# Performance work log

Hardware: AMD Instinct MI355X
Metric: run time of the kernel (lower is better)

The kernel has to match this reference:

```python
import jax, jax.numpy as jnp
import numpy as np

D = 768
NH = 12
HD = D // NH
N_MLP = 3072
LN_EPS = 1e-6


def layer_norm(x, g, b, eps=LN_EPS):
    mu = jnp.mean(x, axis=-1, keepdims=True)
    var = jnp.mean(jnp.square(x - mu), axis=-1, keepdims=True)
    return (x - mu) * jax.lax.rsqrt(var + eps) * g + b


def setup_inputs() -> dict:
    key = jax.random.key(0)
    ks = jax.random.split(key, 6)
    x = jax.random.normal(ks[0], (2, 4096, D), dtype=jnp.float32)
    # torch Linear weights are (out, in); init std=0.02, zero bias
    W_qkv = 0.02 * jax.random.normal(ks[1], (3 * D, D), dtype=jnp.float32)
    b_qkv = jnp.zeros((3 * D,), dtype=jnp.float32)
    W_proj = 0.02 * jax.random.normal(ks[2], (D, D), dtype=jnp.float32)
    b_proj = jnp.zeros((D,), dtype=jnp.float32)
    W1 = 0.02 * jax.random.normal(ks[3], (N_MLP, D), dtype=jnp.float32)
    b1 = jnp.zeros((N_MLP,), dtype=jnp.float32)
    W2 = 0.02 * jax.random.normal(ks[4], (D, N_MLP), dtype=jnp.float32)
    b2 = jnp.zeros((D,), dtype=jnp.float32)
    g1 = jnp.ones((D,), dtype=jnp.float32)
    beta1 = jnp.zeros((D,), dtype=jnp.float32)
    g2 = jnp.ones((D,), dtype=jnp.float32)
    beta2 = jnp.zeros((D,), dtype=jnp.float32)
    return dict(x=x, W_qkv=W_qkv, b_qkv=b_qkv, W_proj=W_proj, b_proj=b_proj,
                W1=W1, b1=b1, W2=W2, b2=b2,
                g1=g1, beta1=beta1, g2=g2, beta2=beta2)


def reference(x, W_qkv, b_qkv, W_proj, b_proj, W1, b1, W2, b2, g1, beta1, g2, beta2):
    B, T, d = x.shape
    scale = HD ** (-0.5)
    # --- attention branch (pre-norm) ---
    h = layer_norm(x, g1, beta1)
    qkv = h @ W_qkv.T + b_qkv                      # [B,T,3d]
    qkv = qkv.reshape(B, T, 3, NH, HD)
    q, k, v = qkv[:, :, 0], qkv[:, :, 1], qkv[:, :, 2]  # [B,T,NH,HD]
    logits = jnp.einsum('bthc,bshc->bhts', q, k) * scale
    attn = jax.nn.softmax(logits, axis=-1)
    out = jnp.einsum('bhts,bshc->bthc', attn, v).reshape(B, T, d)
    out = out @ W_proj.T + b_proj
    x = x + out
    # --- MLP branch (pre-norm) ---
    h = layer_norm(x, g2, beta2)
    h = jax.nn.gelu(h @ W1.T + b1, approximate=False)
    h = h @ W2.T + b2
    return x + h
```

## Files before the change

kernel.cpp:

```cpp
#include <hip/hip_runtime.h>
#include <cmath>

typedef __attribute__((ext_vector_type(4))) float f32x4;
typedef __attribute__((ext_vector_type(16))) float f32x16;
typedef __attribute__((ext_vector_type(8))) __bf16 bf16x8;
typedef __attribute__((ext_vector_type(8))) unsigned short u16x8;
typedef __attribute__((ext_vector_type(4))) unsigned short u16x4;
typedef __attribute__((ext_vector_type(2))) unsigned int u32x2;
typedef __attribute__((ext_vector_type(4))) unsigned int u32x4;

#define DEV __device__ __forceinline__

DEV unsigned short f2b(float v) {
  __bf16 b = (__bf16)v;
  return __builtin_bit_cast(unsigned short, b);
}

DEV unsigned int cvtpk(float lo, float hi) {
  unsigned int r;
  asm("v_cvt_pk_bf16_f32 %0, %1, %2" : "=v"(r) : "v"(lo), "v"(hi));
  return r;
}

DEV float exp2a(float x) {
  float r;
  asm("v_exp_f32 %0, %1" : "=v"(r) : "v"(x));
  return r;
}

DEV void swap32(unsigned int& x, unsigned int& y) {
  asm("v_permlane32_swap_b32 %0, %1" : "+v"(x), "+v"(y));
}

DEV u32x2 tr_b16(const unsigned short* p) {
  u32x2 r;
  asm volatile("ds_read_b64_tr_b16 %0, %1"
               : "=v"(r)
               : "v"((unsigned int)(unsigned long long)p)
               : "memory");
  return r;
}

DEV void gll16(const void* g, const void* l) {
  __builtin_amdgcn_global_load_lds(
      (const __attribute__((address_space(1))) unsigned int*)(unsigned long long)g,
      (__attribute__((address_space(3))) unsigned int*)(unsigned int)(unsigned long long)l,
      16, 0, 0);
}

DEV float bflo(unsigned int u) { return __builtin_bit_cast(float, u << 16); }
DEV float bfhi(unsigned int u) { return __builtin_bit_cast(float, u & 0xFFFF0000u); }

DEV void ln_row(const float* __restrict__ xr, const float* __restrict__ g,
                const float* __restrict__ be, unsigned short* __restrict__ orow, int l) {
  float4 v[3];
  float s = 0.f, sq = 0.f;
#pragma unroll
  for (int j = 0; j < 3; ++j) {
    v[j] = ((const float4*)xr)[l + 64 * j];
    s += v[j].x + v[j].y + v[j].z + v[j].w;
    sq += v[j].x * v[j].x + v[j].y * v[j].y + v[j].z * v[j].z + v[j].w * v[j].w;
  }
#pragma unroll
  for (int m = 1; m < 64; m <<= 1) {
    s += __shfl_xor(s, m);
    sq += __shfl_xor(sq, m);
  }
  float mu = s * (1.f / 768.f);
  float var = sq * (1.f / 768.f) - mu * mu;
  float rs = rsqrtf(var + 1e-6f);
#pragma unroll
  for (int j = 0; j < 3; ++j) {
    int c4 = l + 64 * j;
    float4 gv = ((const float4*)g)[c4];
    float4 bv = ((const float4*)be)[c4];
    u16x4 o = {f2b((v[j].x - mu) * rs * gv.x + bv.x),
               f2b((v[j].y - mu) * rs * gv.y + bv.y),
               f2b((v[j].z - mu) * rs * gv.z + bv.z),
               f2b((v[j].w - mu) * rs * gv.w + bv.w)};
    *(u16x4*)(orow + c4 * 4) = o;
  }
}

__global__ void k_ln(const float* __restrict__ x, const float* __restrict__ g,
                     const float* __restrict__ be, unsigned short* __restrict__ out) {
  int row = blockIdx.x * 4 + (threadIdx.x >> 6);
  int l = threadIdx.x & 63;
  ln_row(x + (size_t)row * 768, g, be, out + (size_t)row * 768, l);
}

__global__ void k_pre(const float* __restrict__ x, const float* __restrict__ g,
                      const float* __restrict__ be, unsigned short* __restrict__ h1,
                      const float* __restrict__ s0, const float* __restrict__ s1,
                      const float* __restrict__ s2, const float* __restrict__ s3,
                      unsigned short* __restrict__ wdst) {
  int bid = blockIdx.x;
  if (bid < 2048) {
    int row = bid * 4 + (threadIdx.x >> 6);
    int l = threadIdx.x & 63;
    ln_row(x + (size_t)row * 768, g, be, h1 + (size_t)row * 768, l);
    return;
  }
  int i = (bid - 2048) * 256 + threadIdx.x;
  const float* s;
  unsigned short* d;
  if (i < 442368) {
    s = s0 + (size_t)i * 4;
    d = wdst + (size_t)i * 4;
  } else if (i < 589824) {
    int j = i - 442368;
    s = s1 + (size_t)j * 4;
    d = wdst + 1769472 + (size_t)j * 4;
  } else if (i < 1179648) {
    int j = i - 589824;
    s = s2 + (size_t)j * 4;
    d = wdst + 2359296 + (size_t)j * 4;
  } else {
    int j = i - 1179648;
    s = s3 + (size_t)j * 4;
    d = wdst + 4718592 + (size_t)j * 4;
  }
  float4 v = *(const float4*)s;
  u16x4 o = {f2b(v.x), f2b(v.y), f2b(v.z), f2b(v.w)};
  *(u16x4*)d = o;
}

template <int MODE, int BM>
__global__ __launch_bounds__(256, 2) void k_gemm(
    const unsigned short* __restrict__ A, const unsigned short* __restrict__ Bw,
    const float* __restrict__ bias, const float* __restrict__ res,
    void* __restrict__ outp, int N, int K) {
  __shared__ unsigned short As[2][BM * 64];
  __shared__ unsigned short Bs[2][128 * 64];
  constexpr int MR = BM / 64;
  constexpr int AI = BM / 32;
  constexpr int LPT = AI + 4;
  const int tid = threadIdx.x;
  const int w = tid >> 6, l = tid & 63;
  const int wr = w >> 1, wc = w & 1;
  const int l31 = l & 31, khalf = l >> 5;
  const int nwg = gridDim.x * gridDim.y;
  const int bid = blockIdx.y * gridDim.x + blockIdx.x;
  const int swz = (bid & 7) * (nwg >> 3) + (bid >> 3);
  const int bx = swz % gridDim.x, by = swz / gridDim.x;
  const int brow = by * BM, bcol = bx * 128;

  auto stage = [&](int buf, int kt) {
#pragma unroll
    for (int i = 0; i < AI; ++i) {
      int c = i * 256 + tid;
      int row = c >> 3, cg = (c & 7) ^ (row & 7);
      gll16(A + (size_t)(brow + row) * K + kt + cg * 8,
            (const char*)&As[buf][0] + (i * 256 + (w << 6)) * 16);
    }
#pragma unroll
    for (int i = 0; i < 4; ++i) {
      int c = i * 256 + tid;
      int row = c >> 3, cg = (c & 7) ^ (row & 7);
      gll16(Bw + (size_t)(bcol + row) * K + kt + cg * 8,
            (const char*)&Bs[buf][0] + (i * 256 + (w << 6)) * 16);
    }
  };

  stage(0, 0);
  if (64 < K) stage(1, 64);
  f32x16 acc[MR][2] = {};
  for (int kt = 0, t = 0; kt < K; kt += 64, ++t) {
    const int cur = t & 1;
    if (kt + 64 < K) {
      if constexpr (LPT == 8)
        asm volatile("s_waitcnt vmcnt(8)" ::: "memory");
      else
        asm volatile("s_waitcnt vmcnt(6)" ::: "memory");
    } else {
      asm volatile("s_waitcnt vmcnt(0)" ::: "memory");
    }
    __builtin_amdgcn_s_barrier();
    __builtin_amdgcn_sched_barrier(0);
    bf16x8 af[MR][4], bfr[2][4];
#pragma unroll
    for (int m = 0; m < MR; ++m) {
      int row = wr * (BM / 2) + m * 32 + l31;
#pragma unroll
      for (int s = 0; s < 4; ++s)
        af[m][s] =
            *(const bf16x8*)&As[cur][row * 64 + (((s * 2 + khalf) ^ (row & 7)) << 3)];
    }
#pragma unroll
    for (int n = 0; n < 2; ++n) {
      int row = wc * 64 + n * 32 + l31;
#pragma unroll
      for (int s = 0; s < 4; ++s)
        bfr[n][s] =
            *(const bf16x8*)&Bs[cur][row * 64 + (((s * 2 + khalf) ^ (row & 7)) << 3)];
    }
    asm volatile("s_waitcnt lgkmcnt(0)" ::: "memory");
    __builtin_amdgcn_sched_barrier(0);
    __builtin_amdgcn_s_barrier();
    if (kt + 128 < K) stage(cur, kt + 128);
    __builtin_amdgcn_s_setprio(1);
#pragma unroll
    for (int s = 0; s < 4; ++s)
#pragma unroll
      for (int m = 0; m < MR; ++m)
#pragma unroll
        for (int n = 0; n < 2; ++n)
          acc[m][n] = __builtin_amdgcn_mfma_f32_32x32x16_bf16(af[m][s], bfr[n][s],
                                                              acc[m][n], 0, 0, 0);
    __builtin_amdgcn_s_setprio(0);
  }
#pragma unroll
  for (int n = 0; n < 2; ++n) {
    int col = bcol + wc * 64 + n * 32 + l31;
    float bv = bias[col];
#pragma unroll
    for (int m = 0; m < MR; ++m) {
      int row0 = brow + wr * (BM / 2) + m * 32 + 4 * khalf;
#pragma unroll
      for (int r = 0; r < 16; ++r) {
        int row = row0 + (r & 3) + 8 * (r >> 2);
        size_t idx = (size_t)row * N + col;
        float v = acc[m][n][r] + bv;
        if (MODE == 0) {
          ((unsigned short*)outp)[idx] = f2b(v);
        } else if (MODE == 1) {
          ((float*)outp)[idx] = v + res[idx];
        } else if (MODE == 2) {
          ((unsigned short*)outp)[idx] = f2b(0.5f * v * (1.f + erff(v * 0.70710678f)));
        } else {
          ((float*)outp)[idx] = v + res[idx];
        }
      }
    }
  }
}

__global__ __launch_bounds__(256, 4) void k_attn(const unsigned short* __restrict__ qkv,
                                                 u32x4* __restrict__ Opk,
                                                 float* __restrict__ ml) {
  __shared__ unsigned short Ks[2][64 * 64];
  __shared__ unsigned short Vs[2][4 * 64 * 16];
  const int tid = threadIdx.x;
  const int w = tid >> 6, l = tid & 63;
  const int lq = l & 31, hi = l >> 5;
  const int p = blockIdx.x;
  const int linear = (p & 7) * 192 + (p >> 3);
  const int bh = linear >> 6, rem = linear & 63;
  const int qt = rem >> 1, half = rem & 1;
  const int b = bh / 12, h = bh % 12;
  const size_t base = (size_t)b * 4096 * 2304;
  const int qbase = qt * 128 + w * 32;
  const int kv0 = half * 2048;

  const float SC = 0.18033688f;
  bf16x8 qb[4];
#pragma unroll
  for (int s = 0; s < 4; ++s) {
    u16x8 raw = *(const u16x8*)(qkv + base + (size_t)(qbase + lq) * 2304 + h * 64 +
                                s * 16 + hi * 8);
    u32x4 pk;
#pragma unroll
    for (int d = 0; d < 4; ++d) {
      float f0 = __builtin_bit_cast(float, (unsigned int)raw[2 * d] << 16) * SC;
      float f1 = __builtin_bit_cast(float, (unsigned int)raw[2 * d + 1] << 16) * SC;
      pk[d] = cvtpk(f0, f1);
    }
    qb[s] = __builtin_bit_cast(bf16x8, pk);
  }

  const unsigned short* pK = qkv + base + (size_t)(kv0 + 16 * w + (l >> 3)) * 2304 + 768 +
                             h * 64 + (((l & 7) ^ ((l >> 3) & 7)) << 3);
  const unsigned short* pV = qkv + base + (size_t)(kv0 + (l >> 1)) * 2304 + 1536 + h * 64 +
                             w * 16 + ((l & 1) << 3);
  const size_t STEP = (size_t)64 * 2304;

  {
    const char* dK = (const char*)&Ks[0][0] + w * 2048;
    const char* dV = (const char*)&Vs[0][0] + w * 2048;
    gll16(pK, dK);
    gll16(pK + 8 * 2304, dK + 1024);
    gll16(pV, dV);
    gll16(pV + 32 * 2304, dV + 1024);
    pK += STEP;
    pV += STEP;
  }

  f32x16 O[2] = {};
  float lrun = 0.f;

  int it = 0;
  for (int t = 0; t < 32; ++t, it ^= 1) {
    asm volatile("s_waitcnt vmcnt(0)" ::: "memory");
    __syncthreads();
    if (t < 31) {
      const char* dK = (const char*)&Ks[it ^ 1][0] + w * 2048;
      const char* dV = (const char*)&Vs[it ^ 1][0] + w * 2048;
      gll16(pK, dK);
      gll16(pK + 8 * 2304, dK + 1024);
      gll16(pV, dV);
      gll16(pV + 32 * 2304, dV + 1024);
      pK += STEP;
      pV += STEP;
    }

    f32x16 st[2] = {{0}, {0}};
    __builtin_amdgcn_s_setprio(1);
#pragma unroll
    for (int kt = 0; kt < 2; ++kt) {
      int key = kt * 32 + lq;
#pragma unroll
      for (int s = 0; s < 4; ++s) {
        bf16x8 ka =
            *(const bf16x8*)&Ks[it][key * 64 + ((s * 16 + hi * 8) ^ ((key & 7) << 3))];
        st[kt] = __builtin_amdgcn_mfma_f32_32x32x16_bf16(ka, qb[s], st[kt], 0, 0, 0);
      }
    }
    __builtin_amdgcn_s_setprio(0);

    float s0 = 0.f, s1 = 0.f, s2 = 0.f, s3 = 0.f;
#pragma unroll
    for (int kt = 0; kt < 2; ++kt) {
#pragma unroll
      for (int r = 0; r < 16; r += 4) {
        float p0 = exp2a(st[kt][r + 0]);
        float p1 = exp2a(st[kt][r + 1]);
        float p2 = exp2a(st[kt][r + 2]);
        float p3 = exp2a(st[kt][r + 3]);
        st[kt][r + 0] = p0;
        st[kt][r + 1] = p1;
        st[kt][r + 2] = p2;
        st[kt][r + 3] = p3;
        s0 += p0;
        s1 += p1;
        s2 += p2;
        s3 += p3;
      }
    }
    float ssum = (s0 + s1) + (s2 + s3);
    lrun += ssum + __shfl_xor(ssum, 32);

    u32x4 pf[4];
#pragma unroll
    for (int kt = 0; kt < 2; ++kt)
#pragma unroll
      for (int h2 = 0; h2 < 2; ++h2) {
        int r0 = h2 * 8;
        unsigned int a0 = cvtpk(st[kt][r0 + 0], st[kt][r0 + 1]);
        unsigned int a1 = cvtpk(st[kt][r0 + 2], st[kt][r0 + 3]);
        unsigned int b0 = cvtpk(st[kt][r0 + 4], st[kt][r0 + 5]);
        unsigned int b1 = cvtpk(st[kt][r0 + 6], st[kt][r0 + 7]);
        swap32(a0, b0);
        swap32(a1, b1);
        pf[kt * 2 + h2] = u32x4{a0, a1, b0, b1};
      }

#pragma unroll
    for (int hb = 0; hb < 2; ++hb) {
      u32x2 vt[4][2];
      const unsigned short* vbase = &Vs[it][(hb * 2 + (lq >> 4)) * 1024 + (lq & 15)];
#pragma unroll
      for (int s = 0; s < 4; ++s)
#pragma unroll
        for (int t2 = 0; t2 < 2; ++t2)
          vt[s][t2] = tr_b16(vbase + ((s * 16 + hi * 8 + t2 * 4) << 4));
      asm volatile("s_waitcnt lgkmcnt(0)" ::: "memory");
      __builtin_amdgcn_sched_barrier(0);
      __builtin_amdgcn_s_setprio(1);
#pragma unroll
      for (int s = 0; s < 4; ++s) {
        u32x4 vv = {vt[s][0].x, vt[s][0].y, vt[s][1].x, vt[s][1].y};
        O[hb] = __builtin_amdgcn_mfma_f32_32x32x16_bf16(
            __builtin_bit_cast(bf16x8, vv), __builtin_bit_cast(bf16x8, pf[s]), O[hb], 0, 0, 0);
      }
      __builtin_amdgcn_s_setprio(0);
    }
  }

  if (hi == 0) ml[(linear * 4 + w) * 32 + lq] = lrun;
#pragma unroll
  for (int hb = 0; hb < 2; ++hb)
#pragma unroll
    for (int v = 0; v < 2; ++v) {
      u32x4 pkv = {cvtpk(O[hb][8 * v + 0], O[hb][8 * v + 1]),
                   cvtpk(O[hb][8 * v + 2], O[hb][8 * v + 3]),
                   cvtpk(O[hb][8 * v + 4], O[hb][8 * v + 5]),
                   cvtpk(O[hb][8 * v + 6], O[hb][8 * v + 7])};
      Opk[((linear * 4 + w) * 4 + hb * 2 + v) * 64 + l] = pkv;
    }
}

__global__ __launch_bounds__(256) void k_merge(const u32x4* __restrict__ Opk,
                                               const float* __restrict__ ml,
                                               unsigned short* __restrict__ out) {
  const int g = blockIdx.x;
  const int bh = g >> 5, qt = g & 31;
  const int b = bh / 12, h = bh % 12;
  const int tid = threadIdx.x;
  const int w = tid >> 6, l = tid & 63;
  const int lq = l & 31, hi = l >> 5;
  const int bidA = bh * 64 + qt * 2;
  const int bidB = bidA + 1;
  float l0 = ml[(bidA * 4 + w) * 32 + lq];
  float l1 = ml[(bidB * 4 + w) * 32 + lq];
  float rl = 1.f / (l0 + l1);
  const int t = qt * 128 + w * 32 + lq;
  unsigned short* orow = out + (size_t)(b * 4096 + t) * 768 + h * 64;
#pragma unroll
  for (int hb = 0; hb < 2; ++hb)
#pragma unroll
    for (int v = 0; v < 2; ++v) {
      u32x4 va = Opk[((bidA * 4 + w) * 4 + hb * 2 + v) * 64 + l];
      u32x4 vb = Opk[((bidB * 4 + w) * 4 + hb * 2 + v) * 64 + l];
      unsigned int dw[4];
#pragma unroll
      for (int d = 0; d < 4; ++d) {
        float lo = (bflo(va[d]) + bflo(vb[d])) * rl;
        float hi2 = (bfhi(va[d]) + bfhi(vb[d])) * rl;
        dw[d] = cvtpk(lo, hi2);
      }
      *(u32x2*)(orow + hb * 32 + 8 * (2 * v) + 4 * hi) = u32x2{dw[0], dw[1]};
      *(u32x2*)(orow + hb * 32 + 8 * (2 * v + 1) + 4 * hi) = u32x2{dw[2], dw[3]};
    }
}

extern "C" void kernel_launch(void* const* d_in, const int* in_sizes, int n_in,
                              void* d_out, int out_size, void* d_ws, size_t ws_size,
                              hipStream_t stream) {
  const float* x = (const float*)d_in[0];
  const float* Wqkv = (const float*)d_in[1];
  const float* bqkv = (const float*)d_in[2];
  const float* Wproj = (const float*)d_in[3];
  const float* bproj = (const float*)d_in[4];
  const float* W1 = (const float*)d_in[5];
  const float* b1 = (const float*)d_in[6];
  const float* W2 = (const float*)d_in[7];
  const float* b2 = (const float*)d_in[8];
  const float* g1 = (const float*)d_in[9];
  const float* be1 = (const float*)d_in[10];
  const float* g2 = (const float*)d_in[11];
  const float* be2 = (const float*)d_in[12];

  char* ws = (char*)d_ws;
  unsigned short* wqkv = (unsigned short*)(ws + 0);
  unsigned short* wproj = (unsigned short*)(ws + 3538944);
  unsigned short* ww1 = (unsigned short*)(ws + 4718592);
  unsigned short* ww2 = (unsigned short*)(ws + 9437184);
  unsigned short* h1 = (unsigned short*)(ws + 14155776);
  unsigned short* qkvb = (unsigned short*)(ws + 26738688);
  unsigned short* attno = (unsigned short*)(ws + 64487424);
  float* x1 = (float*)(ws + 77070336);
  unsigned short* h2 = (unsigned short*)(ws + 102236160);
  unsigned short* m1 = (unsigned short*)(ws + 114819072);
  u32x4* Opk = (u32x4*)m1;
  float* mlbuf = (float*)h1;

  k_pre<<<8960, 256, 0, stream>>>(x, g1, be1, h1, Wqkv, Wproj, W1, W2, wqkv);

  k_gemm<0, 128><<<dim3(18, 64), 256, 0, stream>>>(h1, wqkv, bqkv, nullptr, qkvb, 2304, 768);
  k_attn<<<1536, 256, 0, stream>>>(qkvb, Opk, mlbuf);
  k_merge<<<768, 256, 0, stream>>>(Opk, mlbuf, attno);
  k_gemm<1, 128><<<dim3(6, 64), 256, 0, stream>>>(attno, wproj, bproj, x, x1, 768, 768);
  k_ln<<<2048, 256, 0, stream>>>(x1, g2, be2, h2);
  k_gemm<2, 128><<<dim3(24, 64), 256, 0, stream>>>(h2, ww1, b1, nullptr, m1, 3072, 768);
  k_gemm<3, 128><<<dim3(6, 64), 256, 0, stream>>>(m1, ww2, b2, x1, (float*)d_out, 768, 3072);
}
```

Before: 341.3 us.

## Switch GEMM to 16x16x32 MFMA and use 64-wide N tiles for narrow GEMMs

New measurement: 334.4 us (median of 3 runs). 1.02x faster.

```diff
diff --git a/kernel.cpp b/kernel.cpp
--- a/kernel.cpp
+++ b/kernel.cpp
@@ -125,25 +125,27 @@
   *(u16x4*)d = o;
 }
 
-template <int MODE, int BM>
+template <int MODE, int BM, int BN>
 __global__ __launch_bounds__(256, 2) void k_gemm(
     const unsigned short* __restrict__ A, const unsigned short* __restrict__ Bw,
     const float* __restrict__ bias, const float* __restrict__ res,
     void* __restrict__ outp, int N, int K) {
   __shared__ unsigned short As[2][BM * 64];
-  __shared__ unsigned short Bs[2][128 * 64];
-  constexpr int MR = BM / 64;
+  __shared__ unsigned short Bs[2][BN * 64];
+  constexpr int MR = BM / 32;
+  constexpr int NR = BN / 32;
   constexpr int AI = BM / 32;
-  constexpr int LPT = AI + 4;
+  constexpr int BI = BN / 32;
+  constexpr int LPT = AI + BI;
   const int tid = threadIdx.x;
   const int w = tid >> 6, l = tid & 63;
   const int wr = w >> 1, wc = w & 1;
-  const int l31 = l & 31, khalf = l >> 5;
+  const int lr = l & 15, lg = l >> 4;
   const int nwg = gridDim.x * gridDim.y;
   const int bid = blockIdx.y * gridDim.x + blockIdx.x;
   const int swz = (bid & 7) * (nwg >> 3) + (bid >> 3);
   const int bx = swz % gridDim.x, by = swz / gridDim.x;
-  const int brow = by * BM, bcol = bx * 128;
+  const int brow = by * BM, bcol = bx * BN;
 
   auto stage = [&](int buf, int kt) {
 #pragma unroll
@@ -154,7 +156,7 @@
             (const char*)&As[buf][0] + (i * 256 + (w << 6)) * 16);
     }
 #pragma unroll
-    for (int i = 0; i < 4; ++i) {
+    for (int i = 0; i < BI; ++i) {
       int c = i * 256 + tid;
       int row = c >> 3, cg = (c & 7) ^ (row & 7);
       gll16(Bw + (size_t)(bcol + row) * K + kt + cg * 8,
@@ -164,35 +166,35 @@
 
   stage(0, 0);
   if (64 < K) stage(1, 64);
-  f32x16 acc[MR][2] = {};
+  f32x4 acc[MR][NR] = {};
   for (int kt = 0, t = 0; kt < K; kt += 64, ++t) {
     const int cur = t & 1;
     if (kt + 64 < K) {
       if constexpr (LPT == 8)
         asm volatile("s_waitcnt vmcnt(8)" ::: "memory");
+      else if constexpr (LPT == 6)
+        asm volatile("s_waitcnt vmcnt(6)" ::: "memory");
       else
-        asm volatile("s_waitcnt vmcnt(6)" ::: "memory");
+        asm volatile("s_waitcnt vmcnt(4)" ::: "memory");
     } else {
       asm volatile("s_waitcnt vmcnt(0)" ::: "memory");
     }
     __builtin_amdgcn_s_barrier();
     __builtin_amdgcn_sched_barrier(0);
-    bf16x8 af[MR][4], bfr[2][4];
+    bf16x8 af[MR][2], bfr[NR][2];
 #pragma unroll
     for (int m = 0; m < MR; ++m) {
-      int row = wr * (BM / 2) + m * 32 + l31;
-#pragma unroll
-      for (int s = 0; s < 4; ++s)
-        af[m][s] =
-            *(const bf16x8*)&As[cur][row * 64 + (((s * 2 + khalf) ^ (row & 7)) << 3)];
-    }
-#pragma unroll
-    for (int n = 0; n < 2; ++n) {
-      int row = wc * 64 + n * 32 + l31;
-#pragma unroll
-      for (int s = 0; s < 4; ++s)
-        bfr[n][s] =
-            *(const bf16x8*)&Bs[cur][row * 64 + (((s * 2 + khalf) ^ (row & 7)) << 3)];
+      int row = wr * (BM / 2) + m * 16 + lr;
+#pragma unroll
+      for (int s = 0; s < 2; ++s)
+        af[m][s] = *(const bf16x8*)&As[cur][row * 64 + (((s * 4 + lg) ^ (row & 7)) << 3)];
+    }
+#pragma unroll
+    for (int n = 0; n < NR; ++n) {
+      int row = wc * (BN / 2) + n * 16 + lr;
+#pragma unroll
+      for (int s = 0; s < 2; ++s)
+        bfr[n][s] = *(const bf16x8*)&Bs[cur][row * 64 + (((s * 4 + lg) ^ (row & 7)) << 3)];
     }
     asm volatile("s_waitcnt lgkmcnt(0)" ::: "memory");
     __builtin_amdgcn_sched_barrier(0);
@@ -200,26 +202,25 @@
     if (kt + 128 < K) stage(cur, kt + 128);
     __builtin_amdgcn_s_setprio(1);
 #pragma unroll
-    for (int s = 0; s < 4; ++s)
+    for (int s = 0; s < 2; ++s)
 #pragma unroll
       for (int m = 0; m < MR; ++m)
 #pragma unroll
-        for (int n = 0; n < 2; ++n)
-          acc[m][n] = __builtin_amdgcn_mfma_f32_32x32x16_bf16(af[m][s], bfr[n][s],
-                                                              acc[m][n], 0, 0, 0);
+        for (int n = 0; n < NR; ++n)
+          acc[m][n] =
+              __builtin_amdgcn_mfma_f32_16x16x32_bf16(af[m][s], bfr[n][s], acc[m][n], 0, 0, 0);
     __builtin_amdgcn_s_setprio(0);
   }
 #pragma unroll
-  for (int n = 0; n < 2; ++n) {
-    int col = bcol + wc * 64 + n * 32 + l31;
+  for (int n = 0; n < NR; ++n) {
+    int col = bcol + wc * (BN / 2) + n * 16 + lr;
     float bv = bias[col];
 #pragma unroll
     for (int m = 0; m < MR; ++m) {
-      int row0 = brow + wr * (BM / 2) + m * 32 + 4 * khalf;
-#pragma unroll
-      for (int r = 0; r < 16; ++r) {
-        int row = row0 + (r & 3) + 8 * (r >> 2);
-        size_t idx = (size_t)row * N + col;
+      int row0 = brow + wr * (BM / 2) + m * 16 + lg * 4;
+#pragma unroll
+      for (int r = 0; r < 4; ++r) {
+        size_t idx = (size_t)(row0 + r) * N + col;
         float v = acc[m][n][r] + bv;
         if (MODE == 0) {
           ((unsigned short*)outp)[idx] = f2b(v);
@@ -456,11 +457,11 @@
 
   k_pre<<<8960, 256, 0, stream>>>(x, g1, be1, h1, Wqkv, Wproj, W1, W2, wqkv);
 
-  k_gemm<0, 128><<<dim3(18, 64), 256, 0, stream>>>(h1, wqkv, bqkv, nullptr, qkvb, 2304, 768);
+  k_gemm<0, 128, 128><<<dim3(18, 64), 256, 0, stream>>>(h1, wqkv, bqkv, nullptr, qkvb, 2304, 768);
   k_attn<<<1536, 256, 0, stream>>>(qkvb, Opk, mlbuf);
   k_merge<<<768, 256, 0, stream>>>(Opk, mlbuf, attno);
-  k_gemm<1, 128><<<dim3(6, 64), 256, 0, stream>>>(attno, wproj, bproj, x, x1, 768, 768);
+  k_gemm<1, 128, 64><<<dim3(12, 64), 256, 0, stream>>>(attno, wproj, bproj, x, x1, 768, 768);
   k_ln<<<2048, 256, 0, stream>>>(x1, g2, be2, h2);
-  k_gemm<2, 128><<<dim3(24, 64), 256, 0, stream>>>(h2, ww1, b1, nullptr, m1, 3072, 768);
-  k_gemm<3, 128><<<dim3(6, 64), 256, 0, stream>>>(m1, ww2, b2, x1, (float*)d_out, 768, 3072);
-}
+  k_gemm<2, 128, 128><<<dim3(24, 64), 256, 0, stream>>>(h2, ww1, b1, nullptr, m1, 3072, 768);
+  k_gemm<3, 128, 64><<<dim3(12, 64), 256, 0, stream>>>(m1, ww2, b2, x1, (float*)d_out, 768, 3072);
+}
```
